# Optimization experiments

Measured on AMD Instinct MI355X. Metric: run time of the kernel, lower is better.

The kernel has to match this reference:

```python
import jax, jax.numpy as jnp
import numpy as np

N = 131072   # octree nodes at this depth
K = 27       # 3x3x3 kernel taps
CIN = 32
COUT = 32
EPS = 1e-5   # BatchNorm1d default eps


def setup_inputs() -> dict:
    key = jax.random.key(0)
    k1, k2, k3, k4, k5 = jax.random.split(key, 5)
    data = jax.random.normal(k1, (N, CIN), dtype=jnp.float32)
    # deconv weight: one [Cin, Cout] matrix per kernel tap
    weight = jax.random.normal(k2, (K, CIN, COUT), dtype=jnp.float32) * 0.05
    gamma = 1.0 + 0.1 * jax.random.normal(k3, (COUT,), dtype=jnp.float32)
    beta = 0.1 * jax.random.normal(k4, (COUT,), dtype=jnp.float32)
    # octree neighbor table: for each input node, the K output nodes it scatters into
    neigh = jax.random.randint(k5, (N, K), 0, N, dtype=jnp.int32)
    return {"data": data, "weight": weight, "gamma": gamma, "beta": beta, "neigh": neigh}


def reference(data, weight, gamma, beta, neigh):
    # Sparse transposed conv (stride=1): each node i produces a contribution
    # data[i] @ weight[k] that is scatter-added into output node neigh[i, k].
    contrib = jnp.einsum('ni,kio->nko', data, weight)          # [N, K, Cout]
    out = jax.ops.segment_sum(contrib.reshape(-1, COUT),
                              neigh.reshape(-1),
                              num_segments=N)                   # [N, Cout]
    # BatchNorm1d (training mode: batch statistics over the node dimension)
    mean = jnp.mean(out, axis=0)
    var = jnp.var(out, axis=0)
    y = gamma * (out - mean) * jax.lax.rsqrt(var + EPS) + beta
    # ReLU
    return jnp.maximum(y, 0.0)
```

## Files before the change

### kernel.cpp

```cpp
#include <hip/hip_runtime.h>
#include <hip/hip_bf16.h>
#include <hip/hip_fp16.h>

#define NN 131072
#define KK 27
#define CC 32
#define EPSV 1e-5f

#define WS_STATS 0
#define WS_ACC   256
#define WS_NEEDED ((size_t)WS_ACC + (size_t)NN * CC * 2)

typedef __bf16 bf16x8 __attribute__((ext_vector_type(8)));
typedef short s16x8 __attribute__((ext_vector_type(8)));
typedef float f32x4 __attribute__((ext_vector_type(4)));

__device__ inline unsigned short f2bf(float f) {
    unsigned int u = __float_as_uint(f);
    u += 0x7FFF + ((u >> 16) & 1);
    return (unsigned short)(u >> 16);
}

__global__ __launch_bounds__(256) void scatter_kernel(
    const float* __restrict__ data, const float* __restrict__ weight,
    const int* __restrict__ neigh, __half2* __restrict__ acc2)
{
    __shared__ unsigned short wfrag[KK * 2 * 64 * 8];

    const int tid = threadIdx.x;
    const int lane = tid & 63;
    const int wv = tid >> 6;
    const int node_base = blockIdx.x * 128;

    for (int p = tid; p < KK * 1024; p += 256) {
        const int k  = p >> 10;
        const int ci = (p >> 5) & 31;
        const int c  = p & 31;
        const unsigned short v = f2bf(weight[p]);
        const int chalf = c & 1;
        const int col   = c >> 1;
        const int fl = col | ((ci >> 3) << 4);
        const int j = ci & 7;
        wfrag[(((k << 1) | chalf) * 64 + fl) * 8 + j] = v;
    }

    const int quad = lane >> 4;
    const int m = lane & 15;
    s16x8 afr[2];
    #pragma unroll
    for (int g = 0; g < 2; ++g) {
        const int node = node_base + wv * 32 + g * 16 + m;
        const float* src = data + node * 32 + quad * 8;
        const float4 v0 = *(const float4*)(src);
        const float4 v1 = *(const float4*)(src + 4);
        s16x8 s;
        s[0] = (short)f2bf(v0.x); s[1] = (short)f2bf(v0.y);
        s[2] = (short)f2bf(v0.z); s[3] = (short)f2bf(v0.w);
        s[4] = (short)f2bf(v1.x); s[5] = (short)f2bf(v1.y);
        s[6] = (short)f2bf(v1.z); s[7] = (short)f2bf(v1.w);
        afr[g] = s;
    }

    __syncthreads();

    const int rq = quad << 2;
    const f32x4 zero = {0.f, 0.f, 0.f, 0.f};

    for (int k = 0; k < KK; ++k) {
        int nj[2][4];
        #pragma unroll
        for (int g = 0; g < 2; ++g)
            #pragma unroll
            for (int r = 0; r < 4; ++r) {
                const int node = node_base + wv * 32 + g * 16 + rq + r;
                nj[g][r] = neigh[node * KK + k];
            }
        const s16x8 bs0 = *(const s16x8*)&wfrag[(((k << 1) | 0) * 64 + lane) * 8];
        const s16x8 bs1 = *(const s16x8*)&wfrag[(((k << 1) | 1) * 64 + lane) * 8];
        #pragma unroll
        for (int g = 0; g < 2; ++g) {
            const f32x4 d0 = __builtin_amdgcn_mfma_f32_16x16x32_bf16(
                __builtin_bit_cast(bf16x8, afr[g]), __builtin_bit_cast(bf16x8, bs0),
                zero, 0, 0, 0);
            const f32x4 d1 = __builtin_amdgcn_mfma_f32_16x16x32_bf16(
                __builtin_bit_cast(bf16x8, afr[g]), __builtin_bit_cast(bf16x8, bs1),
                zero, 0, 0, 0);
            #pragma unroll
            for (int r = 0; r < 4; ++r) {
                __half2 v;
                v.x = __float2half(d0[r]);
                v.y = __float2half(d1[r]);
                unsafeAtomicAdd(&acc2[nj[g][r] * 16 + m], v);
            }
        }
    }
}

__global__ __launch_bounds__(256) void stats_kernel(
    const __half2* __restrict__ acc2, float* __restrict__ stats)
{
    __shared__ float ls[16][33], ls2[16][33];
    const int tid = threadIdx.x;
    const int c2 = tid & 15, rg = tid >> 4;
    float sx = 0.f, sy = 0.f, s2x = 0.f, s2y = 0.f;
    const int row0 = blockIdx.x * 512;
    for (int it = 0; it < 32; ++it) {
        const __half2 h = acc2[(row0 + it * 16 + rg) * 16 + c2];
        const float vx = __half2float(h.x), vy = __half2float(h.y);
        sx += vx; sy += vy; s2x += vx * vx; s2y += vy * vy;
    }
    ls[rg][2 * c2] = sx;  ls[rg][2 * c2 + 1] = sy;
    ls2[rg][2 * c2] = s2x; ls2[rg][2 * c2 + 1] = s2y;
    __syncthreads();
    if (tid < 32) {
        float S = 0.f, S2 = 0.f;
        #pragma unroll
        for (int g = 0; g < 16; ++g) { S += ls[g][tid]; S2 += ls2[g][tid]; }
        atomicAdd(&stats[tid], S);
        atomicAdd(&stats[32 + tid], S2);
    }
}

__global__ __launch_bounds__(256) void bn_relu_kernel(
    const __half2* __restrict__ acc2, float* __restrict__ out,
    const float* __restrict__ stats,
    const float* __restrict__ gamma, const float* __restrict__ beta)
{
    __shared__ float sc[32], sh[32];
    const int tid = threadIdx.x;
    if (tid < 32) {
        const float mean = stats[tid] * (1.0f / NN);
        const float var  = stats[32 + tid] * (1.0f / NN) - mean * mean;
        const float s = gamma[tid] * rsqrtf(var + EPSV);
        sc[tid] = s;
        sh[tid] = beta[tid] - mean * s;
    }
    __syncthreads();
    const int idx = blockIdx.x * 256 + tid;
    const int c0 = (idx & 3) << 3;
    const __half2 h4[4] = { acc2[idx * 4], acc2[idx * 4 + 1],
                            acc2[idx * 4 + 2], acc2[idx * 4 + 3] };
    float4 o0, o1;
    o0.x = fmaxf(__half2float(h4[0].x) * sc[c0]     + sh[c0],     0.f);
    o0.y = fmaxf(__half2float(h4[0].y) * sc[c0 + 1] + sh[c0 + 1], 0.f);
    o0.z = fmaxf(__half2float(h4[1].x) * sc[c0 + 2] + sh[c0 + 2], 0.f);
    o0.w = fmaxf(__half2float(h4[1].y) * sc[c0 + 3] + sh[c0 + 3], 0.f);
    o1.x = fmaxf(__half2float(h4[2].x) * sc[c0 + 4] + sh[c0 + 4], 0.f);
    o1.y = fmaxf(__half2float(h4[2].y) * sc[c0 + 5] + sh[c0 + 5], 0.f);
    o1.z = fmaxf(__half2float(h4[3].x) * sc[c0 + 6] + sh[c0 + 6], 0.f);
    o1.w = fmaxf(__half2float(h4[3].y) * sc[c0 + 7] + sh[c0 + 7], 0.f);
    ((float4*)out)[idx * 2]     = o0;
    ((float4*)out)[idx * 2 + 1] = o1;
}

__global__ __launch_bounds__(256) void scatter_f32_kernel(
    const float* __restrict__ data, const float* __restrict__ weight,
    const int* __restrict__ neigh, float* __restrict__ out)
{
    __shared__ unsigned short wfrag[KK * 2 * 64 * 8];
    const int tid = threadIdx.x;
    const int lane = tid & 63;
    const int wv = tid >> 6;
    const int node_base = blockIdx.x * 128;
    for (int p = tid; p < KK * 1024; p += 256) {
        const int k  = p >> 10;
        const int ci = (p >> 5) & 31;
        const int c  = p & 31;
        const unsigned short v = f2bf(weight[p]);
        const int chalf = c >> 4;
        const int fl = (c & 15) | ((ci >> 3) << 4);
        const int j = ci & 7;
        wfrag[(((k << 1) | chalf) * 64 + fl) * 8 + j] = v;
    }
    const int quad = lane >> 4;
    const int m = lane & 15;
    s16x8 afr[2];
    #pragma unroll
    for (int g = 0; g < 2; ++g) {
        const int node = node_base + wv * 32 + g * 16 + m;
        const float* src = data + node * 32 + quad * 8;
        const float4 v0 = *(const float4*)(src);
        const float4 v1 = *(const float4*)(src + 4);
        s16x8 s;
        s[0] = (short)f2bf(v0.x); s[1] = (short)f2bf(v0.y);
        s[2] = (short)f2bf(v0.z); s[3] = (short)f2bf(v0.w);
        s[4] = (short)f2bf(v1.x); s[5] = (short)f2bf(v1.y);
        s[6] = (short)f2bf(v1.z); s[7] = (short)f2bf(v1.w);
        afr[g] = s;
    }
    __syncthreads();
    const int rq = quad << 2;
    const f32x4 zero = {0.f, 0.f, 0.f, 0.f};
    for (int k = 0; k < KK; ++k) {
        int nj[2][4];
        #pragma unroll
        for (int g = 0; g < 2; ++g)
            #pragma unroll
            for (int r = 0; r < 4; ++r) {
                const int node = node_base + wv * 32 + g * 16 + rq + r;
                nj[g][r] = neigh[node * KK + k];
            }
        #pragma unroll
        for (int ch = 0; ch < 2; ++ch) {
            const s16x8 bs = *(const s16x8*)&wfrag[((((k << 1) | ch)) * 64 + lane) * 8];
            const bf16x8 bfr = __builtin_bit_cast(bf16x8, bs);
            const int c = (ch << 4) | m;
            #pragma unroll
            for (int g = 0; g < 2; ++g) {
                f32x4 a2 = __builtin_amdgcn_mfma_f32_16x16x32_bf16(
                    __builtin_bit_cast(bf16x8, afr[g]), bfr, zero, 0, 0, 0);
                #pragma unroll
                for (int r = 0; r < 4; ++r)
                    __hip_atomic_fetch_add(&out[nj[g][r] * 32 + c], a2[r],
                                           __ATOMIC_RELAXED, __HIP_MEMORY_SCOPE_AGENT);
            }
        }
    }
}

__global__ __launch_bounds__(256) void stats_f32_kernel(
    const float* __restrict__ out, float* __restrict__ stats)
{
    __shared__ float ls[256], ls2[256];
    const int tid = threadIdx.x;
    const int c = tid & 31, rg = tid >> 5;
    float s = 0.f, s2 = 0.f;
    const int row0 = blockIdx.x * 512;
    for (int it = 0; it < 64; ++it) {
        const float v = out[(row0 + it * 8 + rg) * 32 + c];
        s += v; s2 += v * v;
    }
    ls[tid] = s; ls2[tid] = s2;
    __syncthreads();
    if (tid < 32) {
        float S = 0.f, S2 = 0.f;
        #pragma unroll
        for (int r = 0; r < 8; ++r) { S += ls[r * 32 + tid]; S2 += ls2[r * 32 + tid]; }
        atomicAdd(&stats[tid], S);
        atomicAdd(&stats[32 + tid], S2);
    }
}

__global__ __launch_bounds__(256) void bn_relu_f32_kernel(
    float* __restrict__ out, const float* __restrict__ stats,
    const float* __restrict__ gamma, const float* __restrict__ beta)
{
    __shared__ float sc[32], sh[32];
    const int tid = threadIdx.x;
    if (tid < 32) {
        const float mean = stats[tid] * (1.0f / NN);
        const float var  = stats[32 + tid] * (1.0f / NN) - mean * mean;
        const float s = gamma[tid] * rsqrtf(var + EPSV);
        sc[tid] = s;
        sh[tid] = beta[tid] - mean * s;
    }
    __syncthreads();
    const int idx = blockIdx.x * 256 + tid;
    float4 v = ((float4*)out)[idx];
    const int cb = (idx & 7) << 2;
    v.x = fmaxf(v.x * sc[cb]     + sh[cb],     0.f);
    v.y = fmaxf(v.y * sc[cb + 1] + sh[cb + 1], 0.f);
    v.z = fmaxf(v.z * sc[cb + 2] + sh[cb + 2], 0.f);
    v.w = fmaxf(v.w * sc[cb + 3] + sh[cb + 3], 0.f);
    ((float4*)out)[idx] = v;
}

extern "C" void kernel_launch(void* const* d_in, const int* in_sizes, int n_in,
                              void* d_out, int out_size, void* d_ws, size_t ws_size,
                              hipStream_t stream) {
    const float* data   = (const float*)d_in[0];
    const float* weight = (const float*)d_in[1];
    const float* gamma  = (const float*)d_in[2];
    const float* beta   = (const float*)d_in[3];
    const int*   neigh  = (const int*)d_in[4];
    float* out = (float*)d_out;
    char* ws = (char*)d_ws;
    float* stats = (float*)(ws + WS_STATS);

    if (ws_size >= WS_NEEDED) {
        __half2* acc2 = (__half2*)(ws + WS_ACC);
        hipMemsetAsync(ws, 0, WS_NEEDED, stream);
        scatter_kernel<<<NN / 128, 256, 0, stream>>>(data, weight, neigh, acc2);
        stats_kernel<<<NN / 512, 256, 0, stream>>>(acc2, stats);
        bn_relu_kernel<<<(NN * CC / 8) / 256, 256, 0, stream>>>(acc2, out, stats, gamma, beta);
    } else {
        hipMemsetAsync(out, 0, (size_t)NN * CC * sizeof(float), stream);
        hipMemsetAsync(stats, 0, 64 * sizeof(float), stream);
        scatter_f32_kernel<<<NN / 128, 256, 0, stream>>>(data, weight, neigh, out);
        stats_f32_kernel<<<NN / 512, 256, 0, stream>>>(out, stats);
        bn_relu_f32_kernel<<<(NN * CC / 4) / 256, 256, 0, stream>>>(out, stats, gamma, beta);
    }
}
```

Measured before the change: 272.1 us.

## Fuse scatter, stats and BN-ReLU into one cooperative kernel with grid syncs

New measurement: 389.5 us. 43.2% more time.

```diff
diff --git a/kernel.cpp b/kernel.cpp
--- a/kernel.cpp
+++ b/kernel.cpp
@@ -1,12 +1,18 @@
 #include <hip/hip_runtime.h>
 #include <hip/hip_bf16.h>
 #include <hip/hip_fp16.h>
+#include <hip/hip_cooperative_groups.h>
+
+namespace cg = cooperative_groups;
 
 #define NN 131072
 #define KK 27
 #define CC 32
 #define EPSV 1e-5f
 
+#define NBLK 512
+#define NPB  256
+
 #define WS_STATS 0
 #define WS_ACC   256
 #define WS_NEEDED ((size_t)WS_ACC + (size_t)NN * CC * 2)
@@ -21,16 +27,19 @@
     return (unsigned short)(u >> 16);
 }
 
-__global__ __launch_bounds__(256) void scatter_kernel(
+__global__ __launch_bounds__(256) void fused_kernel(
     const float* __restrict__ data, const float* __restrict__ weight,
-    const int* __restrict__ neigh, __half2* __restrict__ acc2)
+    const int* __restrict__ neigh, __half2* __restrict__ acc2,
+    float* __restrict__ stats, float* __restrict__ out,
+    const float* __restrict__ gamma, const float* __restrict__ beta)
 {
-    __shared__ unsigned short wfrag[KK * 2 * 64 * 8];
+    cg::grid_group grid = cg::this_grid();
+    __shared__ __align__(16) unsigned short wfrag[KK * 2 * 64 * 8];
 
     const int tid = threadIdx.x;
-    const int lane = tid & 63;
-    const int wv = tid >> 6;
-    const int node_base = blockIdx.x * 128;
+    const int bid = blockIdx.x;
+    const int lane = tid & 63, wv = tid >> 6;
+    const int quad = lane >> 4, m = lane & 15, rq = quad << 2;
 
     for (int p = tid; p < KK * 1024; p += 256) {
         const int k  = p >> 10;
@@ -43,114 +52,117 @@
         const int j = ci & 7;
         wfrag[(((k << 1) | chalf) * 64 + fl) * 8 + j] = v;
     }
-
-    const int quad = lane >> 4;
-    const int m = lane & 15;
-    s16x8 afr[2];
-    #pragma unroll
-    for (int g = 0; g < 2; ++g) {
-        const int node = node_base + wv * 32 + g * 16 + m;
-        const float* src = data + node * 32 + quad * 8;
-        const float4 v0 = *(const float4*)(src);
-        const float4 v1 = *(const float4*)(src + 4);
-        s16x8 s;
-        s[0] = (short)f2bf(v0.x); s[1] = (short)f2bf(v0.y);
-        s[2] = (short)f2bf(v0.z); s[3] = (short)f2bf(v0.w);
-        s[4] = (short)f2bf(v1.x); s[5] = (short)f2bf(v1.y);
-        s[6] = (short)f2bf(v1.z); s[7] = (short)f2bf(v1.w);
-        afr[g] = s;
-    }
-
     __syncthreads();
 
-    const int rq = quad << 2;
     const f32x4 zero = {0.f, 0.f, 0.f, 0.f};
-
-    for (int k = 0; k < KK; ++k) {
-        int nj[2][4];
-        #pragma unroll
-        for (int g = 0; g < 2; ++g)
-            #pragma unroll
-            for (int r = 0; r < 4; ++r) {
-                const int node = node_base + wv * 32 + g * 16 + rq + r;
-                nj[g][r] = neigh[node * KK + k];
+    for (int chunk = 0; chunk < 2; ++chunk) {
+        const int node_base = bid * NPB + chunk * 128;
+        s16x8 afr[2];
+        #pragma unroll
+        for (int g = 0; g < 2; ++g) {
+            const int node = node_base + wv * 32 + g * 16 + m;
+            const float* src = data + node * 32 + quad * 8;
+            const float4 v0 = *(const float4*)(src);
+            const float4 v1 = *(const float4*)(src + 4);
+            s16x8 s;
+            s[0] = (short)f2bf(v0.x); s[1] = (short)f2bf(v0.y);
+            s[2] = (short)f2bf(v0.z); s[3] = (short)f2bf(v0.w);
+            s[4] = (short)f2bf(v1.x); s[5] = (short)f2bf(v1.y);
+            s[6] = (short)f2bf(v1.z); s[7] = (short)f2bf(v1.w);
+            afr[g] = s;
+        }
+        for (int k = 0; k < KK; ++k) {
+            int nj[2][4];
+            #pragma unroll
+            for (int g = 0; g < 2; ++g)
+                #pragma unroll
+                for (int r = 0; r < 4; ++r) {
+                    const int node = node_base + wv * 32 + g * 16 + rq + r;
+                    nj[g][r] = neigh[node * KK + k];
+                }
+            const s16x8 bs0 = *(const s16x8*)&wfrag[(((k << 1) | 0) * 64 + lane) * 8];
+            const s16x8 bs1 = *(const s16x8*)&wfrag[(((k << 1) | 1) * 64 + lane) * 8];
+            #pragma unroll
+            for (int g = 0; g < 2; ++g) {
+                const f32x4 d0 = __builtin_amdgcn_mfma_f32_16x16x32_bf16(
+                    __builtin_bit_cast(bf16x8, afr[g]), __builtin_bit_cast(bf16x8, bs0),
+                    zero, 0, 0, 0);
+                const f32x4 d1 = __builtin_amdgcn_mfma_f32_16x16x32_bf16(
+                    __builtin_bit_cast(bf16x8, afr[g]), __builtin_bit_cast(bf16x8, bs1),
+                    zero, 0, 0, 0);
+                #pragma unroll
+                for (int r = 0; r < 4; ++r) {
+                    __half2 v;
+                    v.x = __float2half(d0[r]);
+                    v.y = __float2half(d1[r]);
+                    unsafeAtomicAdd(&acc2[nj[g][r] * 16 + m], v);
+                }
             }
-        const s16x8 bs0 = *(const s16x8*)&wfrag[(((k << 1) | 0) * 64 + lane) * 8];
-        const s16x8 bs1 = *(const s16x8*)&wfrag[(((k << 1) | 1) * 64 + lane) * 8];
-        #pragma unroll
-        for (int g = 0; g < 2; ++g) {
-            const f32x4 d0 = __builtin_amdgcn_mfma_f32_16x16x32_bf16(
-                __builtin_bit_cast(bf16x8, afr[g]), __builtin_bit_cast(bf16x8, bs0),
-                zero, 0, 0, 0);
-            const f32x4 d1 = __builtin_amdgcn_mfma_f32_16x16x32_bf16(
-                __builtin_bit_cast(bf16x8, afr[g]), __builtin_bit_cast(bf16x8, bs1),
-                zero, 0, 0, 0);
-            #pragma unroll
-            for (int r = 0; r < 4; ++r) {
-                __half2 v;
-                v.x = __float2half(d0[r]);
-                v.y = __float2half(d1[r]);
-                unsafeAtomicAdd(&acc2[nj[g][r] * 16 + m], v);
+        }
+    }
+
+    grid.sync();
+
+    {
+        float* red = (float*)wfrag;
+        const int c2 = tid & 15, rg = tid >> 4;
+        float sx = 0.f, sy = 0.f, s2x = 0.f, s2y = 0.f;
+        const int row0 = bid * NPB;
+        for (int it = 0; it < 16; ++it) {
+            const __half2 h = acc2[(row0 + it * 16 + rg) * 16 + c2];
+            const float vx = __half2float(h.x), vy = __half2float(h.y);
+            sx += vx; sy += vy; s2x += vx * vx; s2y += vy * vy;
+        }
+        red[(0 * 16 + rg) * 33 + 2 * c2]     = sx;
+        red[(0 * 16 + rg) * 33 + 2 * c2 + 1] = sy;
+        red[(1 * 16 + rg) * 33 + 2 * c2]     = s2x;
+        red[(1 * 16 + rg) * 33 + 2 * c2 + 1] = s2y;
+        __syncthreads();
+        if (tid < 32) {
+            float S = 0.f, S2 = 0.f;
+            #pragma unroll
+            for (int g = 0; g < 16; ++g) {
+                S  += red[(0 * 16 + g) * 33 + tid];
+                S2 += red[(1 * 16 + g) * 33 + tid];
             }
-        }
-    }
-}
-
-__global__ __launch_bounds__(256) void stats_kernel(
-    const __half2* __restrict__ acc2, float* __restrict__ stats)
-{
-    __shared__ float ls[16][33], ls2[16][33];
-    const int tid = threadIdx.x;
-    const int c2 = tid & 15, rg = tid >> 4;
-    float sx = 0.f, sy = 0.f, s2x = 0.f, s2y = 0.f;
-    const int row0 = blockIdx.x * 512;
-    for (int it = 0; it < 32; ++it) {
-        const __half2 h = acc2[(row0 + it * 16 + rg) * 16 + c2];
-        const float vx = __half2float(h.x), vy = __half2float(h.y);
-        sx += vx; sy += vy; s2x += vx * vx; s2y += vy * vy;
-    }
-    ls[rg][2 * c2] = sx;  ls[rg][2 * c2 + 1] = sy;
-    ls2[rg][2 * c2] = s2x; ls2[rg][2 * c2 + 1] = s2y;
-    __syncthreads();
-    if (tid < 32) {
-        float S = 0.f, S2 = 0.f;
-        #pragma unroll
-        for (int g = 0; g < 16; ++g) { S += ls[g][tid]; S2 += ls2[g][tid]; }
-        atomicAdd(&stats[tid], S);
-        atomicAdd(&stats[32 + tid], S2);
-    }
-}
-
-__global__ __launch_bounds__(256) void bn_relu_kernel(
-    const __half2* __restrict__ acc2, float* __restrict__ out,
-    const float* __restrict__ stats,
-    const float* __restrict__ gamma, const float* __restrict__ beta)
-{
-    __shared__ float sc[32], sh[32];
-    const int tid = threadIdx.x;
-    if (tid < 32) {
-        const float mean = stats[tid] * (1.0f / NN);
-        const float var  = stats[32 + tid] * (1.0f / NN) - mean * mean;
-        const float s = gamma[tid] * rsqrtf(var + EPSV);
-        sc[tid] = s;
-        sh[tid] = beta[tid] - mean * s;
-    }
-    __syncthreads();
-    const int idx = blockIdx.x * 256 + tid;
-    const int c0 = (idx & 3) << 3;
-    const __half2 h4[4] = { acc2[idx * 4], acc2[idx * 4 + 1],
-                            acc2[idx * 4 + 2], acc2[idx * 4 + 3] };
-    float4 o0, o1;
-    o0.x = fmaxf(__half2float(h4[0].x) * sc[c0]     + sh[c0],     0.f);
-    o0.y = fmaxf(__half2float(h4[0].y) * sc[c0 + 1] + sh[c0 + 1], 0.f);
-    o0.z = fmaxf(__half2float(h4[1].x) * sc[c0 + 2] + sh[c0 + 2], 0.f);
-    o0.w = fmaxf(__half2float(h4[1].y) * sc[c0 + 3] + sh[c0 + 3], 0.f);
-    o1.x = fmaxf(__half2float(h4[2].x) * sc[c0 + 4] + sh[c0 + 4], 0.f);
-    o1.y = fmaxf(__half2float(h4[2].y) * sc[c0 + 5] + sh[c0 + 5], 0.f);
-    o1.z = fmaxf(__half2float(h4[3].x) * sc[c0 + 6] + sh[c0 + 6], 0.f);
-    o1.w = fmaxf(__half2float(h4[3].y) * sc[c0 + 7] + sh[c0 + 7], 0.f);
-    ((float4*)out)[idx * 2]     = o0;
-    ((float4*)out)[idx * 2 + 1] = o1;
+            atomicAdd(&stats[tid], S);
+            atomicAdd(&stats[32 + tid], S2);
+        }
+    }
+
+    grid.sync();
+
+    {
+        float* sc = (float*)wfrag;
+        float* sh = sc + 32;
+        __syncthreads();
+        if (tid < 32) {
+            const float mean = stats[tid] * (1.0f / NN);
+            const float var  = stats[32 + tid] * (1.0f / NN) - mean * mean;
+            const float s = gamma[tid] * rsqrtf(var + EPSV);
+            sc[tid] = s;
+            sh[tid] = beta[tid] - mean * s;
+        }
+        __syncthreads();
+        #pragma unroll
+        for (int p = 0; p < 4; ++p) {
+            const int idx = bid * 1024 + p * 256 + tid;
+            const int c0 = (idx & 3) << 3;
+            const __half2 h0 = acc2[idx * 4],     h1 = acc2[idx * 4 + 1];
+            const __half2 h2 = acc2[idx * 4 + 2], h3 = acc2[idx * 4 + 3];
+            float4 o0, o1;
+            o0.x = fmaxf(__half2float(h0.x) * sc[c0]     + sh[c0],     0.f);
+            o0.y = fmaxf(__half2float(h0.y) * sc[c0 + 1] + sh[c0 + 1], 0.f);
+            o0.z = fmaxf(__half2float(h1.x) * sc[c0 + 2] + sh[c0 + 2], 0.f);
+            o0.w = fmaxf(__half2float(h1.y) * sc[c0 + 3] + sh[c0 + 3], 0.f);
+            o1.x = fmaxf(__half2float(h2.x) * sc[c0 + 4] + sh[c0 + 4], 0.f);
+            o1.y = fmaxf(__half2float(h2.y) * sc[c0 + 5] + sh[c0 + 5], 0.f);
+            o1.z = fmaxf(__half2float(h3.x) * sc[c0 + 6] + sh[c0 + 6], 0.f);
+            o1.w = fmaxf(__half2float(h3.y) * sc[c0 + 7] + sh[c0 + 7], 0.f);
+            ((float4*)out)[idx * 2]     = o0;
+            ((float4*)out)[idx * 2 + 1] = o1;
+        }
+    }
 }
 
 __global__ __launch_bounds__(256) void scatter_f32_kernel(
@@ -280,9 +292,10 @@
     if (ws_size >= WS_NEEDED) {
         __half2* acc2 = (__half2*)(ws + WS_ACC);
         hipMemsetAsync(ws, 0, WS_NEEDED, stream);
-        scatter_kernel<<<NN / 128, 256, 0, stream>>>(data, weight, neigh, acc2);
-        stats_kernel<<<NN / 512, 256, 0, stream>>>(acc2, stats);
-        bn_relu_kernel<<<(NN * CC / 8) / 256, 256, 0, stream>>>(acc2, out, stats, gamma, beta);
+        void* args[8] = {(void*)&data, (void*)&weight, (void*)&neigh, (void*)&acc2,
+                         (void*)&stats, (void*)&out, (void*)&gamma, (void*)&beta};
+        hipLaunchCooperativeKernel((const void*)fused_kernel, dim3(NBLK), dim3(256),
+                                   args, 0, stream);
     } else {
         hipMemsetAsync(out, 0, (size_t)NN * CC * sizeof(float), stream);
         hipMemsetAsync(stats, 0, 64 * sizeof(float), stream);
```
